# Kernel optimization log

Hardware: AMD Instinct MI355X
Metric: run time of the kernel (lower is better)

Reference implementation:

```python
import jax, jax.numpy as jnp
import numpy as np

IN_DIM = 64
OUT_DIM = 64
N_MODES = 32


def setup_inputs() -> dict:
    key = jax.random.key(0)
    k_x, k_w0, k_w1 = jax.random.split(key, 3)
    x = jax.random.normal(k_x, (32, IN_DIM, 128, 128), dtype=jnp.float32)
    # xavier_normal_ on tensor of shape (in, out, modes, 2): fan_in = out*modes*2, fan_out = in*modes*2? 
    # torch treats dim0 as fan_out-ish; exact init scale is irrelevant for correctness baselines,
    # so use a matching gaussian std = sqrt(2/(in_dim+out_dim)).
    std = float(np.sqrt(2.0 / (IN_DIM + OUT_DIM)))
    w0 = std * jax.random.normal(k_w0, (IN_DIM, OUT_DIM, N_MODES, 2), dtype=jnp.float32)
    w1 = std * jax.random.normal(k_w1, (IN_DIM, OUT_DIM, N_MODES, 2), dtype=jnp.float32)
    return {"x": x, "w0": w0, "w1": w1}


def reference(x, w0, w1):
    B, I, M, N = x.shape
    n_modes = w0.shape[2]

    # ---- width (last-axis) branch ----
    x_fty = jnp.fft.rfft(x, axis=-1, norm='ortho')                      # [B, I, M, N//2+1]
    wc0 = w0[..., 0] + 1j * w0[..., 1]                                  # [I, O, n_modes]
    low_y = jnp.einsum('bixy,ioy->boxy', x_fty[..., :n_modes], wc0)     # [B, O, M, n_modes]
    out_ft_y = jnp.pad(low_y, ((0, 0), (0, 0), (0, 0), (0, N // 2 + 1 - n_modes)))
    xy = jnp.fft.irfft(out_ft_y, n=N, axis=-1, norm='ortho')            # [B, O, M, N]

    # ---- height (second-to-last axis) branch ----
    x_ftx = jnp.fft.rfft(x, axis=-2, norm='ortho')                      # [B, I, M//2+1, N]
    wc1 = w1[..., 0] + 1j * w1[..., 1]                                  # [I, O, n_modes]
    low_x = jnp.einsum('bixy,iox->boxy', x_ftx[:, :, :n_modes, :], wc1)  # [B, O, n_modes, N]
    out_ft_x = jnp.pad(low_x, ((0, 0), (0, 0), (0, M // 2 + 1 - n_modes), (0, 0)))
    xx = jnp.fft.irfft(out_ft_x, n=M, axis=-2, norm='ortho')            # [B, O, M, N]

    return xx + xy
```

## Files before the change

### kernel.cpp

```cpp
#include <hip/hip_runtime.h>


typedef _Float16 half8  __attribute__((ext_vector_type(8)));
typedef _Float16 half4v __attribute__((ext_vector_type(4)));
typedef _Float16 half2v __attribute__((ext_vector_type(2)));
typedef float    floatx4 __attribute__((ext_vector_type(4)));

#define TWO_PI_OVER_128 0.049087385212340517f

__device__ __forceinline__ unsigned int packh2(float a, float b) {
    half2v h; h[0] = (_Float16)a; h[1] = (_Float16)b;
    return __builtin_bit_cast(unsigned int, h);
}
__device__ __forceinline__ half8  ash8(uint4 u) { return __builtin_bit_cast(half8, u); }
__device__ __forceinline__ half4v ash4(uint2 u) { return __builtin_bit_cast(half4v, u); }

#define MFMA_K16(A,B,C) __builtin_amdgcn_mfma_f32_16x16x16f16((A),(B),(C),0,0,0)

#define YS_PK 324
#define YS_PR 20

template<int BR>
__global__ __launch_bounds__(1024, 4) void spectral(const float* __restrict__ x,
                                                    const float* __restrict__ wt,
                                                    float* __restrict__ out)
{
    __shared__ uint4 Ubuf[36864 / 16];
    __shared__ unsigned short Ys[32 * YS_PK];

    unsigned short* Xs = (unsigned short*)Ubuf;
    unsigned int*   Zs = (unsigned int*)Ubuf;

    const int tid  = threadIdx.x;
    const int wv   = tid >> 6;
    const int mrow = tid & 15;
    const int quad = (tid >> 4) & 3;
    const int bx   = blockIdx.x;
    const int b    = bx >> 3;
    const int tile = bx & 7;

    const long xb = (long)b * 1048576 + (BR == 0 ? tile * 2048 : tile * 16);
    const long ob = xb;

    const int kptile = wv & 3;
    half8 Ff[4];
#pragma unroll
    for (int s = 0; s < 4; ++s)
#pragma unroll
        for (int j = 0; j < 8; ++j) {
            int d  = s * 32 + quad * 8 + j;
            int kp = kptile * 16 + mrow;
            int k  = kp >> 1;
            float ang = TWO_PI_OVER_128 * (float)((k * d) & 127);
            float v = (kp & 1) ? -sinf(ang) : cosf(ang);
            Ff[s][j] = (_Float16)v;
        }

    floatx4 acc[2][8];
#pragma unroll
    for (int kk = 0; kk < 2; ++kk)
#pragma unroll
        for (int m = 0; m < 8; ++m)
            acc[kk][m] = (floatx4){0.f, 0.f, 0.f, 0.f};

    const float* wbase = wt + (quad * 2) * 4096 + (mrow >> 1) * 64 + wv * 4;
    const int a_im = mrow & 1;

    if (BR == 0) {
#pragma unroll
        for (int p = 0; p < 4; ++p) {
            int idx = p * 1024 + tid;
            int col = idx >> 5, dg = idx & 31;
            int i = col >> 4, t = col & 15;
            const float4 v = *(const float4*)(x + xb + (long)i * 16384 + t * 128 + dg * 4);
            *(uint2*)&Xs[col * 136 + dg * 4] = make_uint2(packh2(v.x, v.y), packh2(v.z, v.w));
        }
    } else {
#pragma unroll
        for (int p = 0; p < 4; ++p) {
            int i  = (tid >> 9) + p * 2;
            int d  = (tid >> 2) & 127;
            int tq = (tid & 3) * 4;
            const float4 v = *(const float4*)(x + xb + (long)i * 16384 + d * 128 + tq);
            int colb = i * 16 + tq;
            Xs[(colb + 0) * 136 + d] = __builtin_bit_cast(unsigned short, (_Float16)v.x);
            Xs[(colb + 1) * 136 + d] = __builtin_bit_cast(unsigned short, (_Float16)v.y);
            Xs[(colb + 2) * 136 + d] = __builtin_bit_cast(unsigned short, (_Float16)v.z);
            Xs[(colb + 3) * 136 + d] = __builtin_bit_cast(unsigned short, (_Float16)v.w);
        }
    }
    __syncthreads();

    for (int c = 0; c < 8; ++c) {
        float4 pf[4];
        if (c < 7) {
            if (BR == 0) {
#pragma unroll
                for (int p = 0; p < 4; ++p) {
                    int idx = p * 1024 + tid;
                    int col = idx >> 5, dg = idx & 31;
                    int i = col >> 4, t = col & 15;
                    pf[p] = *(const float4*)(x + xb + (long)((c + 1) * 8 + i) * 16384 + t * 128 + dg * 4);
                }
            } else {
#pragma unroll
                for (int p = 0; p < 4; ++p) {
                    int i  = (tid >> 9) + p * 2;
                    int d  = (tid >> 2) & 127;
                    int tq = (tid & 3) * 4;
                    pf[p] = *(const float4*)(x + xb + (long)((c + 1) * 8 + i) * 16384 + d * 128 + tq);
                }
            }
        }

#pragma unroll
        for (int cc = 0; cc < 2; ++cc) {
            int i = (wv >> 2) * 2 + cc;
            floatx4 y4 = {0.f, 0.f, 0.f, 0.f};
#pragma unroll
            for (int s = 0; s < 4; ++s) {
                uint4 bv = *(const uint4*)&Xs[(i * 16 + mrow) * 136 + s * 32 + quad * 8];
                y4 = __builtin_amdgcn_mfma_f32_16x16x32_f16(Ff[s], ash8(bv), y4, 0, 0, 0);
            }
            int k0 = kptile * 8 + quad * 2;
            unsigned int* yw = (unsigned int*)Ys;
            yw[(k0    ) * (YS_PK / 2) + mrow * (YS_PR / 2) + i] = packh2(y4[0], y4[1]);
            yw[(k0 + 1) * (YS_PK / 2) + mrow * (YS_PR / 2) + i] = packh2(y4[2], y4[3]);
        }
        __syncthreads();

        {
            half4v bf0 = ash4(*(const uint2*)&Ys[(wv * 2    ) * YS_PK + mrow * YS_PR + quad * 4]);
            half4v bf1 = ash4(*(const uint2*)&Ys[(wv * 2 + 1) * YS_PK + mrow * YS_PR + quad * 4]);
            const float* wc = wbase + c * 32768;
#pragma unroll
            for (int m = 0; m < 8; ++m) {
                const float4 wA = *(const float4*)(wc + m * 512);
                const float4 wB = *(const float4*)(wc + 4096 + m * 512);
                float s00 = a_im ? wA.y :  wA.x;
                float s01 = a_im ? wA.x : -wA.y;
                float s02 = a_im ? wB.y :  wB.x;
                float s03 = a_im ? wB.x : -wB.y;
                float s10 = a_im ? wA.w :  wA.z;
                float s11 = a_im ? wA.z : -wA.w;
                float s12 = a_im ? wB.w :  wB.z;
                float s13 = a_im ? wB.z : -wB.w;
                uint2 a0u = make_uint2(packh2(s00, s01), packh2(s02, s03));
                uint2 a1u = make_uint2(packh2(s10, s11), packh2(s12, s13));
                acc[0][m] = MFMA_K16(ash4(a0u), bf0, acc[0][m]);
                acc[1][m] = MFMA_K16(ash4(a1u), bf1, acc[1][m]);
            }
        }

        if (c < 7) {
            if (BR == 0) {
#pragma unroll
                for (int p = 0; p < 4; ++p) {
                    int idx = p * 1024 + tid;
                    int col = idx >> 5, dg = idx & 31;
                    *(uint2*)&Xs[col * 136 + dg * 4] =
                        make_uint2(packh2(pf[p].x, pf[p].y), packh2(pf[p].z, pf[p].w));
                }
            } else {
#pragma unroll
                for (int p = 0; p < 4; ++p) {
                    int d  = (tid >> 2) & 127;
                    int tq = (tid & 3) * 4;
                    int colb = ((tid >> 9) + p * 2) * 16 + tq;
                    Xs[(colb + 0) * 136 + d] = __builtin_bit_cast(unsigned short, (_Float16)pf[p].x);
                    Xs[(colb + 1) * 136 + d] = __builtin_bit_cast(unsigned short, (_Float16)pf[p].y);
                    Xs[(colb + 2) * 136 + d] = __builtin_bit_cast(unsigned short, (_Float16)pf[p].z);
                    Xs[(colb + 3) * 136 + d] = __builtin_bit_cast(unsigned short, (_Float16)pf[p].w);
                }
            }
        }
        __syncthreads();
    }

    const int dt  = wv & 7;
    const int ctb = (wv >> 3) * 8;
    const int dp  = dt * 16 + mrow;
    half8 Gf[2];
#pragma unroll
    for (int s = 0; s < 2; ++s)
#pragma unroll
        for (int j = 0; j < 8; ++j) {
            int kp = s * 32 + quad * 8 + j;
            int k  = kp >> 1;
            float ang = TWO_PI_OVER_128 * (float)((k * dp) & 127);
            float v;
            if (kp == 0)      v = 1.f / 128.f;
            else if (kp == 1) v = 0.f;
            else v = (kp & 1) ? -(2.f / 128.f) * sinf(ang) : (2.f / 128.f) * cosf(ang);
            Gf[s][j] = (_Float16)v;
        }

    for (int q = 0; q < 4; ++q) {
        __syncthreads();
#pragma unroll
        for (int mm = 0; mm < 2; ++mm) {
            const int m = q * 2 + mm;
#pragma unroll
            for (int kk = 0; kk < 2; ++kk) {
                const int slot = (wv * 2 + kk) ^ (quad * 8);
                const int col  = (mm * 8 + quad * 2) * 16 + mrow;
                Zs[ col       * 36 + slot] = packh2(acc[kk][m][0], acc[kk][m][1]);
                Zs[(col + 16) * 36 + slot] = packh2(acc[kk][m][2], acc[kk][m][3]);
            }
        }
        __syncthreads();

#pragma unroll
        for (int cc = 0; cc < 8; ++cc) {
            const int ct  = ctb + cc;
            const int col = ct * 16 + mrow;
            const int swz = (ct & 6) << 2;
            floatx4 o4 = {0.f, 0.f, 0.f, 0.f};
#pragma unroll
            for (int s = 0; s < 2; ++s) {
                uint4 zv = *(const uint4*)&Zs[col * 36 + ((s * 16 + quad * 4) ^ swz)];
                o4 = __builtin_amdgcn_mfma_f32_16x16x32_f16(Gf[s], ash8(zv), o4, 0, 0, 0);
            }
            const int oo = q * 16 + ct;
            const int t  = mrow;
            const int db = dt * 16 + quad * 4;
            if (BR == 0) {
                __builtin_nontemporal_store(o4, (floatx4*)(out + ob + (long)oo * 16384 + t * 128 + db));
            } else {
                float* p = out + ob + (long)oo * 16384 + (long)db * 128 + t;
                unsafeAtomicAdd(p,       o4[0]);
                unsafeAtomicAdd(p + 128, o4[1]);
                unsafeAtomicAdd(p + 256, o4[2]);
                unsafeAtomicAdd(p + 384, o4[3]);
            }
        }
    }
}

extern "C" void kernel_launch(void* const* d_in, const int* in_sizes, int n_in,
                              void* d_out, int out_size, void* d_ws, size_t ws_size,
                              hipStream_t stream) {
    const float* x  = (const float*)d_in[0];
    const float* w0 = (const float*)d_in[1];
    const float* w1 = (const float*)d_in[2];
    float* out = (float*)d_out;

    dim3 grid(256);
    dim3 block(1024);

    spectral<0><<<grid, block, 0, stream>>>(x, w0, out);
    spectral<1><<<grid, block, 0, stream>>>(x, w1, out);
}
```

Baseline: 558.1 us.

## Pre-pack spectral weights into fp16 MFMA-fragment layout in a prep kernel

Adds a small kernel that converts both complex weight tensors once per call into fp16 A-fragments laid out per lane in the order the MFMA loop consumes them, stored in workspace. The main kernel then does one coalesced uint2 load per fragment instead of strided float4 loads followed by selects, negation and packing. The forward DFT stage is also moved ahead of the next-chunk prefetch inside the loop. The cost is an extra launch and a workspace round trip.

```diff
diff --git a/kernel.cpp b/kernel.cpp
--- a/kernel.cpp
+++ b/kernel.cpp
@@ -20,9 +20,36 @@
 #define YS_PK 324
 #define YS_PR 20
 
+__global__ __launch_bounds__(256) void w2expand(const float* __restrict__ w0,
+                                                const float* __restrict__ w1,
+                                                uint2* __restrict__ W2h)
+{
+    int g = blockIdx.x * 256 + threadIdx.x;
+    const float* w = (g >> 17) ? w1 : w0;
+    int e    = g & 131071;
+    int lane = e & 63;
+    int m    = (e >> 6) & 7;
+    int c    = (e >> 9) & 7;
+    int k    = e >> 12;
+    int mrow = lane & 15, q = lane >> 4;
+    int o  = (m * 16 + mrow) >> 1;
+    int oc = mrow & 1;
+    unsigned int h2[2];
+#pragma unroll
+    for (int hp = 0; hp < 2; ++hp) {
+        int i = c * 8 + q * 2 + hp;
+        const float* wp = w + ((i * 64 + o) * 32 + k) * 2;
+        float re = wp[0], im = wp[1];
+        float v0 = oc ? im : re;
+        float v1 = oc ? re : -im;
+        h2[hp] = packh2(v0, v1);
+    }
+    W2h[g] = make_uint2(h2[0], h2[1]);
+}
+
 template<int BR>
 __global__ __launch_bounds__(1024, 4) void spectral(const float* __restrict__ x,
-                                                    const float* __restrict__ wt,
+                                                    const uint2* __restrict__ w2,
                                                     float* __restrict__ out)
 {
     __shared__ uint4 Ubuf[36864 / 16];
@@ -33,6 +60,7 @@
 
     const int tid  = threadIdx.x;
     const int wv   = tid >> 6;
+    const int lane = tid & 63;
     const int mrow = tid & 15;
     const int quad = (tid >> 4) & 3;
     const int bx   = blockIdx.x;
@@ -62,9 +90,6 @@
 #pragma unroll
         for (int m = 0; m < 8; ++m)
             acc[kk][m] = (floatx4){0.f, 0.f, 0.f, 0.f};
-
-    const float* wbase = wt + (quad * 2) * 4096 + (mrow >> 1) * 64 + wv * 4;
-    const int a_im = mrow & 1;
 
     if (BR == 0) {
 #pragma unroll
@@ -92,6 +117,22 @@
     __syncthreads();
 
     for (int c = 0; c < 8; ++c) {
+#pragma unroll
+        for (int cc = 0; cc < 2; ++cc) {
+            int i = (wv >> 2) * 2 + cc;
+            floatx4 y4 = {0.f, 0.f, 0.f, 0.f};
+#pragma unroll
+            for (int s = 0; s < 4; ++s) {
+                uint4 bv = *(const uint4*)&Xs[(i * 16 + mrow) * 136 + s * 32 + quad * 8];
+                y4 = __builtin_amdgcn_mfma_f32_16x16x32_f16(Ff[s], ash8(bv), y4, 0, 0, 0);
+            }
+            int k0 = kptile * 8 + quad * 2;
+            unsigned int* yw = (unsigned int*)Ys;
+            yw[(k0    ) * (YS_PK / 2) + mrow * (YS_PR / 2) + i] = packh2(y4[0], y4[1]);
+            yw[(k0 + 1) * (YS_PK / 2) + mrow * (YS_PR / 2) + i] = packh2(y4[2], y4[3]);
+        }
+        __syncthreads();
+
         float4 pf[4];
         if (c < 7) {
             if (BR == 0) {
@@ -113,40 +154,14 @@
             }
         }
 
-#pragma unroll
-        for (int cc = 0; cc < 2; ++cc) {
-            int i = (wv >> 2) * 2 + cc;
-            floatx4 y4 = {0.f, 0.f, 0.f, 0.f};
-#pragma unroll
-            for (int s = 0; s < 4; ++s) {
-                uint4 bv = *(const uint4*)&Xs[(i * 16 + mrow) * 136 + s * 32 + quad * 8];
-                y4 = __builtin_amdgcn_mfma_f32_16x16x32_f16(Ff[s], ash8(bv), y4, 0, 0, 0);
-            }
-            int k0 = kptile * 8 + quad * 2;
-            unsigned int* yw = (unsigned int*)Ys;
-            yw[(k0    ) * (YS_PK / 2) + mrow * (YS_PR / 2) + i] = packh2(y4[0], y4[1]);
-            yw[(k0 + 1) * (YS_PK / 2) + mrow * (YS_PR / 2) + i] = packh2(y4[2], y4[3]);
-        }
-        __syncthreads();
-
         {
             half4v bf0 = ash4(*(const uint2*)&Ys[(wv * 2    ) * YS_PK + mrow * YS_PR + quad * 4]);
             half4v bf1 = ash4(*(const uint2*)&Ys[(wv * 2 + 1) * YS_PK + mrow * YS_PR + quad * 4]);
-            const float* wc = wbase + c * 32768;
+            const uint2* wp = w2 + (((2 * wv) * 8 + c) * 8) * 64 + lane;
 #pragma unroll
             for (int m = 0; m < 8; ++m) {
-                const float4 wA = *(const float4*)(wc + m * 512);
-                const float4 wB = *(const float4*)(wc + 4096 + m * 512);
-                float s00 = a_im ? wA.y :  wA.x;
-                float s01 = a_im ? wA.x : -wA.y;
-                float s02 = a_im ? wB.y :  wB.x;
-                float s03 = a_im ? wB.x : -wB.y;
-                float s10 = a_im ? wA.w :  wA.z;
-                float s11 = a_im ? wA.z : -wA.w;
-                float s12 = a_im ? wB.w :  wB.z;
-                float s13 = a_im ? wB.z : -wB.w;
-                uint2 a0u = make_uint2(packh2(s00, s01), packh2(s02, s03));
-                uint2 a1u = make_uint2(packh2(s10, s11), packh2(s12, s13));
+                uint2 a0u = wp[m * 64];
+                uint2 a1u = wp[m * 64 + 4096];
                 acc[0][m] = MFMA_K16(ash4(a0u), bf0, acc[0][m]);
                 acc[1][m] = MFMA_K16(ash4(a1u), bf1, acc[1][m]);
             }
@@ -245,9 +260,13 @@
     const float* w1 = (const float*)d_in[2];
     float* out = (float*)d_out;
 
+    uint2* W2h = (uint2*)d_ws;
+
+    w2expand<<<dim3(1024), dim3(256), 0, stream>>>(w0, w1, W2h);
+
     dim3 grid(256);
     dim3 block(1024);
 
-    spectral<0><<<grid, block, 0, stream>>>(x, w0, out);
-    spectral<1><<<grid, block, 0, stream>>>(x, w1, out);
-}
+    spectral<0><<<grid, block, 0, stream>>>(x, W2h,          out);
+    spectral<1><<<grid, block, 0, stream>>>(x, W2h + 131072, out);
+}
```

Result: slower. 577.9 us (+3.6%).
